# Kernel optimization log

Hardware: AMD Instinct MI355X
Metric: run time of the kernel (lower is better)

## Reference

```python
import jax, jax.numpy as jnp
import numpy as np

D = 2048
NUM_HEADS = 16
HEAD_DIM = D // NUM_HEADS
B, T = 4, 2048
NEG = -1e9


def setup_inputs() -> dict:
    key = jax.random.key(0)
    ks = jax.random.split(key, 6)
    X = jax.random.normal(ks[0], (B, T, D), dtype=jnp.float32)
    # additive causal mask, broadcast over batch and heads
    causal = jnp.tril(jnp.ones((T, T), dtype=jnp.float32))
    mask = jnp.where(causal == 1, 0.0, NEG)[None, None, :, :]
    scale = np.sqrt(2.0 / D).astype(np.float32)
    wq_w = jax.random.normal(ks[1], (D, D), dtype=jnp.float32) * scale
    wk_w = jax.random.normal(ks[2], (D, D), dtype=jnp.float32) * scale
    wv_w = jax.random.normal(ks[3], (D, D), dtype=jnp.float32) * scale
    wo_w = jax.random.normal(ks[4], (D, D), dtype=jnp.float32) * scale
    zeros = jnp.zeros((D,), dtype=jnp.float32)
    return {
        "X": X, "mask": mask,
        "wq_w": wq_w, "wq_b": zeros,
        "wk_w": wk_w, "wk_b": zeros,
        "wv_w": wv_w, "wv_b": zeros,
        "wo_w": wo_w, "wo_b": zeros,
    }


def reference(X, mask, wq_w, wq_b, wk_w, wk_b, wv_w, wv_b, wo_w, wo_b):
    b, t, d = X.shape
    # project and split heads: [b, h, t, hd]
    def proj(w, bias):
        return (X @ w + bias).reshape(b, t, NUM_HEADS, HEAD_DIM).transpose(0, 2, 1, 3)
    Q = proj(wq_w, wq_b)
    K = proj(wk_w, wk_b)
    V = proj(wv_w, wv_b)
    scores = jnp.einsum("bhqd,bhkd->bhqk", Q, K) / np.sqrt(HEAD_DIM).astype(X.dtype)
    scores = scores + mask
    A = jax.nn.softmax(scores, axis=-1)
    ctx = jnp.einsum("bhqk,bhkd->bhqd", A, V)  # [b, h, t, hd]
    ctx = ctx.transpose(0, 2, 1, 3).reshape(b, t, d)
    return ctx @ wo_w + wo_b
```

## Files before the change

### kernel.cpp

```cpp
#include <hip/hip_runtime.h>
#include <stdint.h>

#define DMODEL 2048
#define NH 16
#define HD 128
#define BATCH 4
#define SEQ 2048
#define MTOT (BATCH * SEQ)
#define LOG2E 1.44269504088896340736f

typedef __bf16 bf16x8 __attribute__((ext_vector_type(8)));
typedef float floatx4 __attribute__((ext_vector_type(4)));

__device__ __forceinline__ uint16_t f2b(float f) {
    union { float f; uint32_t i; } v; v.f = f;
    uint32_t r = v.i + 0x7fffu + ((v.i >> 16) & 1u);
    return (uint16_t)(r >> 16);
}

#define GLD16(gp, lp)                                                          \
    __builtin_amdgcn_global_load_lds(                                          \
        (__attribute__((address_space(1))) unsigned int*)(gp),                 \
        (__attribute__((address_space(3))) unsigned int*)(lp), 16, 0, 0)

#define WAITVMC(N) asm volatile("s_waitcnt vmcnt(" #N ")" ::: "memory")
#define WAITLGKM0                                                              \
    do {                                                                       \
        asm volatile("s_waitcnt lgkmcnt(0)" ::: "memory");                     \
        __builtin_amdgcn_sched_barrier(0);                                     \
    } while (0)

__global__ __launch_bounds__(256) void cvt_bf16(const float* __restrict__ in,
                                                uint16_t* __restrict__ out, int n) {
    const int i = (blockIdx.x * 256 + threadIdx.x) * 8;
    if (i >= n) return;
    const float4 a = *(const float4*)(in + i);
    const float4 b = *(const float4*)(in + i + 4);
    uint16_t v[8] __attribute__((aligned(16))) = {
        f2b(a.x), f2b(a.y), f2b(a.z), f2b(a.w),
        f2b(b.x), f2b(b.y), f2b(b.z), f2b(b.w)};
    *(uint4*)(out + i) = *(const uint4*)v;
}

__global__ __launch_bounds__(256) void tr_wf(const float* __restrict__ in,
                                             uint16_t* __restrict__ out) {
    __shared__ float t[64 * 69];
    const int tid = threadIdx.x;
    const int r0 = blockIdx.y * 64, c0 = blockIdx.x * 64;
    const int rr = tid >> 2, c16 = (tid & 3) << 4;
#pragma unroll
    for (int j = 0; j < 4; j++)
        *(float4*)&t[rr * 69 + c16 + j * 4] =
            *(const float4*)(in + (size_t)(r0 + rr) * DMODEL + c0 + c16 + j * 4);
    __syncthreads();
    const int oc = tid >> 2, r16 = (tid & 3) << 4;
    uint16_t v[16] __attribute__((aligned(16)));
#pragma unroll
    for (int j = 0; j < 16; j++) v[j] = f2b(t[(r16 + j) * 69 + oc]);
    uint16_t* o = out + (size_t)(c0 + oc) * DMODEL + r0 + r16;
    *(uint4*)o = *(const uint4*)v;
    *(uint4*)(o + 8) = *(const uint4*)(v + 8);
}

__global__ __launch_bounds__(512, 2) void gemm256(const uint16_t* __restrict__ A,
                                                  const uint16_t* __restrict__ Bt,
                                                  const float* __restrict__ bias,
                                                  void* __restrict__ Cout,
                                                  float scale, int mode, int tld) {
    __shared__ __attribute__((aligned(16))) uint16_t As[2][32 * 512];
    __shared__ __attribute__((aligned(16))) uint16_t Bs[2][32 * 512];

    const int tid = threadIdx.x, lane = tid & 63, w = tid >> 6;
    const int wr = w >> 2, wc = w & 3;
    const int col = lane & 15, quad = lane >> 4;

    const int nwg = gridDim.x, cpx = nwg >> 3;
    const int swz = ((int)blockIdx.x & 7) * cpx + ((int)blockIdx.x >> 3);
    const long m0 = (long)(swz >> 3) * 256;
    const long n0 = (long)(swz & 7) * 256;

    const uint16_t* Ab = A + (m0 + col) * (size_t)DMODEL + quad * 8;
    const uint16_t* Bb = Bt + (n0 + col) * (size_t)DMODEL + quad * 8;
    const int g0 = w * 2, g1 = w * 2 + 1;

#define STG_A(bf, kt, kk)                                                      \
    do {                                                                       \
        GLD16(Ab + (size_t)(g0 * 16) * DMODEL + (kt) * 64 + (kk) * 32,         \
              &As[bf][(g0 * 2 + (kk)) * 512]);                                 \
        GLD16(Ab + (size_t)(g1 * 16) * DMODEL + (kt) * 64 + (kk) * 32,         \
              &As[bf][(g1 * 2 + (kk)) * 512]);                                 \
    } while (0)
#define STG_B(bf, kt, kk)                                                      \
    do {                                                                       \
        GLD16(Bb + (size_t)(g0 * 16) * DMODEL + (kt) * 64 + (kk) * 32,         \
              &Bs[bf][(g0 * 2 + (kk)) * 512]);                                 \
        GLD16(Bb + (size_t)(g1 * 16) * DMODEL + (kt) * 64 + (kk) * 32,         \
              &Bs[bf][(g1 * 2 + (kk)) * 512]);                                 \
    } while (0)

    floatx4 acc[8][4];
#pragma unroll
    for (int m = 0; m < 8; m++)
#pragma unroll
        for (int n = 0; n < 4; n++) acc[m][n] = (floatx4){0.f, 0.f, 0.f, 0.f};

    const int NT = DMODEL / 64;
    STG_A(0, 0, 0); STG_B(0, 0, 0);
    STG_A(0, 0, 1); STG_B(0, 0, 1);
    STG_A(1, 1, 0); STG_B(1, 1, 0);
    WAITVMC(8);
    __builtin_amdgcn_s_barrier();

    bf16x8 afr[4], bfr[4];

#define PHASE(MS, KK, READB, STAGE_STMT, TAILW)                                \
    do {                                                                       \
        if (READB) {                                                           \
            _Pragma("unroll") for (int n = 0; n < 4; n++)                      \
                bfr[n] = *(const bf16x8*)&Bs[cur][((wc * 4 + n) * 2 + (KK)) *  \
                                                     512 + lane * 8];          \
        }                                                                      \
        _Pragma("unroll") for (int m = 0; m < 4; m++)                          \
            afr[m] = *(const bf16x8*)&As[cur][((wr * 8 + (MS)*4 + m) * 2 +     \
                                               (KK)) * 512 + lane * 8];        \
        STAGE_STMT;                                                            \
        __builtin_amdgcn_s_barrier();                                          \
        WAITLGKM0;                                                             \
        __builtin_amdgcn_s_setprio(1);                                         \
        _Pragma("unroll") for (int m = 0; m < 4; m++)                          \
            _Pragma("unroll") for (int n = 0; n < 4; n++)                      \
                acc[(MS)*4 + m][n] = __builtin_amdgcn_mfma_f32_16x16x32_bf16(  \
                    afr[m], bfr[n], acc[(MS)*4 + m][n], 0, 0, 0);              \
        __builtin_amdgcn_s_setprio(0);                                         \
        TAILW;                                                                 \
        __builtin_amdgcn_s_barrier();                                          \
    } while (0)

#pragma unroll 1
    for (int t = 0; t < NT; ++t) {
        const int cur = t & 1, nxt = cur ^ 1;
        PHASE(0, 0, 1, { if (t + 1 < NT) STG_A(nxt, t + 1, 1); }, {});
        PHASE(1, 0, 0, { if (t + 1 < NT) STG_B(nxt, t + 1, 1); },
              { if (t == NT - 1) { WAITVMC(0); } else { WAITVMC(8); } });
        PHASE(0, 1, 1, { if (t + 2 < NT) STG_A(cur, t + 2, 0); }, {});
        PHASE(1, 1, 0, { if (t + 2 < NT) STG_B(cur, t + 2, 0); },
              { if (t == NT - 2) { WAITVMC(2); }
                else if (t < NT - 2) { WAITVMC(8); } });
    }
#undef PHASE
#undef STG_A
#undef STG_B

    float bv[4];
#pragma unroll
    for (int n = 0; n < 4; n++) bv[n] = bias[n0 + wc * 64 + n * 16 + col];
#pragma unroll
    for (int m = 0; m < 8; m++) {
        const long row = m0 + wr * 128 + m * 16 + quad * 4;
#pragma unroll
        for (int n = 0; n < 4; n++) {
            const long cc = n0 + wc * 64 + n * 16 + col;
            if (mode == 2) {
                uint16_t tmp[4] __attribute__((aligned(8)));
#pragma unroll
                for (int r = 0; r < 4; r++)
                    tmp[r] = f2b((acc[m][n][r] + bv[n]) * scale);
                *(uint2*)&((uint16_t*)Cout)[(size_t)cc * tld + row] =
                    *(const uint2*)tmp;
            } else {
#pragma unroll
                for (int r = 0; r < 4; r++) {
                    const float v = (acc[m][n][r] + bv[n]) * scale;
                    const long idx = (row + r) * DMODEL + cc;
                    if (mode == 1) ((float*)Cout)[idx] = v;
                    else           ((uint16_t*)Cout)[idx] = f2b(v);
                }
            }
        }
    }
}

__global__ __launch_bounds__(256, 2) void gemm(const uint16_t* __restrict__ A,
                                               const uint16_t* __restrict__ Bt,
                                               const float* __restrict__ bias,
                                               void* __restrict__ Cout,
                                               float scale, int mode, int tld) {
    __shared__ __attribute__((aligned(16))) uint16_t As[128 * 32];
    __shared__ __attribute__((aligned(16))) uint16_t Bs[128 * 32];
    const int tid = threadIdx.x, lane = tid & 63, w = tid >> 6;
    const int wr = w >> 1, wc = w & 1;
    const int col = lane & 15, quad = lane >> 4;
    const long m0 = (long)blockIdx.y * 128, n0 = (long)blockIdx.x * 128;

    floatx4 acc[4][4];
#pragma unroll
    for (int i = 0; i < 4; i++)
#pragma unroll
        for (int j = 0; j < 4; j++) acc[i][j] = (floatx4){0.f, 0.f, 0.f, 0.f};

    const int srow = tid >> 2, sc = (tid & 3) << 3;
    const uint16_t* Ag0 = A + (m0 + srow) * DMODEL + sc;
    const uint16_t* Bg0 = Bt + (n0 + srow) * DMODEL + sc;
    const long rstep = (long)64 * DMODEL;
    uint16_t* AsW = &As[w * 512];
    uint16_t* BsW = &Bs[w * 512];

    for (int kt = 0; kt < DMODEL; kt += 32) {
        GLD16(Ag0 + kt, AsW);
        GLD16(Ag0 + rstep + kt, AsW + 2048);
        GLD16(Bg0 + kt, BsW);
        GLD16(Bg0 + rstep + kt, BsW + 2048);
        __syncthreads();
        bf16x8 af[4], bfr[4];
#pragma unroll
        for (int i = 0; i < 4; i++)
            af[i] = *(const bf16x8*)&As[(wr * 64 + i * 16 + col) * 32 + quad * 8];
#pragma unroll
        for (int j = 0; j < 4; j++)
            bfr[j] = *(const bf16x8*)&Bs[(wc * 64 + j * 16 + col) * 32 + quad * 8];
#pragma unroll
        for (int i = 0; i < 4; i++)
#pragma unroll
            for (int j = 0; j < 4; j++)
                acc[i][j] = __builtin_amdgcn_mfma_f32_16x16x32_bf16(af[i], bfr[j],
                                                                    acc[i][j], 0, 0, 0);
        __syncthreads();
    }

    float bv[4];
#pragma unroll
    for (int j = 0; j < 4; j++) bv[j] = bias[n0 + wc * 64 + j * 16 + col];
#pragma unroll
    for (int i = 0; i < 4; i++) {
        const long row = m0 + wr * 64 + i * 16 + quad * 4;
#pragma unroll
        for (int j = 0; j < 4; j++) {
            const long cc = n0 + wc * 64 + j * 16 + col;
            if (mode == 2) {
                uint16_t tmp[4] __attribute__((aligned(8)));
#pragma unroll
                for (int r = 0; r < 4; r++)
                    tmp[r] = f2b((acc[i][j][r] + bv[j]) * scale);
                *(uint2*)&((uint16_t*)Cout)[(size_t)cc * tld + row] =
                    *(const uint2*)tmp;
            } else {
#pragma unroll
                for (int r = 0; r < 4; r++) {
                    const float v = (acc[i][j][r] + bv[j]) * scale;
                    const long idx = (row + r) * DMODEL + cc;
                    if (mode == 1) ((float*)Cout)[idx] = v;
                    else           ((uint16_t*)Cout)[idx] = f2b(v);
                }
            }
        }
    }
}

__global__ __launch_bounds__(256, 2) void flash(uint16_t* __restrict__ QO,
                                                const uint16_t* __restrict__ Kp,
                                                const uint16_t* __restrict__ Vt,
                                                int vld) {
    __shared__ __attribute__((aligned(16))) uint16_t Ks[16 * 512];
    __shared__ __attribute__((aligned(16))) uint16_t Vs[16 * 512];
    __shared__ __attribute__((aligned(16))) uint16_t Ps[4][32 * 88];

    const int tid = threadIdx.x, lane = tid & 63, w = tid >> 6;
    const int col = lane & 15, quad = lane >> 4;
    const int h = blockIdx.y & 15, b = blockIdx.y >> 4;
    const size_t brow = (size_t)b * SEQ;

    const uint16_t* kbase = Kp + brow * DMODEL + h * HD;
    const uint16_t* vtbase = Vt + (size_t)(h * HD) * vld + brow;
    const uint16_t* kg0 = kbase + (size_t)(w * 16 + col) * DMODEL + quad * 8;
    const uint16_t* vg0 = vtbase + (size_t)(w * 32 + col) * vld + quad * 8;

    for (int half = 0; half < 2; ++half) {
        const int qi = half ? (int)blockIdx.x : (15 - (int)blockIdx.x);
        const int q0 = qi * 128;
        uint16_t* qbase = QO + (brow + q0 + w * 32) * DMODEL + h * HD;

        bf16x8 qf[2][4];
#pragma unroll
        for (int i = 0; i < 2; i++)
#pragma unroll
            for (int kk = 0; kk < 4; kk++)
                qf[i][kk] = *(const bf16x8*)(qbase + (size_t)(i * 16 + col) * DMODEL +
                                             kk * 32 + quad * 8);

        floatx4 accO[2][8];
#pragma unroll
        for (int i = 0; i < 2; i++)
#pragma unroll
            for (int jd = 0; jd < 8; jd++) accO[i][jd] = (floatx4){0.f, 0.f, 0.f, 0.f};
        float mrun[2][4], lrun[2][4];
#pragma unroll
        for (int i = 0; i < 2; i++)
#pragma unroll
            for (int r = 0; r < 4; r++) { mrun[i][r] = -1e30f; lrun[i][r] = 0.f; }

        const int nkt = 2 * qi + 2;

        uint4 kv[4], vv4[4];
        {
#pragma unroll
            for (int p = 0; p < 4; p++)
                kv[p] = *(const uint4*)(kg0 + p * 32);
#pragma unroll
            for (int s = 0; s < 2; s++)
#pragma unroll
                for (int k2 = 0; k2 < 2; k2++)
                    vv4[s * 2 + k2] =
                        *(const uint4*)(vg0 + (size_t)s * 16 * vld + k2 * 32);
        }

        for (int ki = 0; ki < nkt; ki++) {
            const int key0 = ki * 64;
#pragma unroll
            for (int p = 0; p < 4; p++)
                *(uint4*)&Ks[(w * 4 + p) * 512 + lane * 8] = kv[p];
#pragma unroll
            for (int s = 0; s < 2; s++)
#pragma unroll
                for (int k2 = 0; k2 < 2; k2++)
                    *(uint4*)&Vs[((w * 2 + s) * 2 + k2) * 512 + lane * 8] =
                        vv4[s * 2 + k2];
            __syncthreads();

            if (ki + 1 < nkt) {
                const size_t koff = (size_t)(key0 + 64);
#pragma unroll
                for (int p = 0; p < 4; p++)
                    kv[p] = *(const uint4*)(kg0 + koff * DMODEL + p * 32);
#pragma unroll
                for (int s = 0; s < 2; s++)
#pragma unroll
                    for (int k2 = 0; k2 < 2; k2++)
                        vv4[s * 2 + k2] = *(const uint4*)(vg0 + (size_t)s * 16 * vld +
                                                          koff + k2 * 32);
            }

            floatx4 s[2][4];
            __builtin_amdgcn_s_setprio(1);
#pragma unroll
            for (int i = 0; i < 2; i++)
#pragma unroll
                for (int jk = 0; jk < 4; jk++) {
                    floatx4 a = (floatx4){0.f, 0.f, 0.f, 0.f};
#pragma unroll
                    for (int kk = 0; kk < 4; kk++) {
                        bf16x8 bb = *(const bf16x8*)&Ks[(jk * 4 + kk) * 512 + lane * 8];
                        a = __builtin_amdgcn_mfma_f32_16x16x32_bf16(qf[i][kk], bb, a, 0, 0, 0);
                    }
                    s[i][jk] = a;
                }
            __builtin_amdgcn_s_setprio(0);

            if (key0 + 63 > q0 + w * 32) {
#pragma unroll
                for (int i = 0; i < 2; i++) {
                    const int qb = q0 + w * 32 + i * 16 + quad * 4;
#pragma unroll
                    for (int jk = 0; jk < 4; jk++) {
                        const int key = key0 + jk * 16 + col;
#pragma unroll
                        for (int r = 0; r < 4; r++)
                            if (key > qb + r) s[i][jk][r] = -1e30f;
                    }
                }
            }

            float alpha[2][4];
#pragma unroll
            for (int i = 0; i < 2; i++)
#pragma unroll
                for (int r = 0; r < 4; r++) {
                    float mx = s[i][0][r];
#pragma unroll
                    for (int jk = 1; jk < 4; jk++) mx = fmaxf(mx, s[i][jk][r]);
                    mx = fmaxf(mx, __shfl_xor(mx, 1, 64));
                    mx = fmaxf(mx, __shfl_xor(mx, 2, 64));
                    mx = fmaxf(mx, __shfl_xor(mx, 4, 64));
                    mx = fmaxf(mx, __shfl_xor(mx, 8, 64));
                    mx = fmaxf(mx, mrun[i][r]);
                    alpha[i][r] = exp2f((mrun[i][r] - mx) * LOG2E);
                    mrun[i][r] = mx;
                }
#pragma unroll
            for (int i = 0; i < 2; i++)
#pragma unroll
                for (int r = 0; r < 4; r++) {
                    float psum = 0.f;
#pragma unroll
                    for (int jk = 0; jk < 4; jk++) {
                        const float p = exp2f((s[i][jk][r] - mrun[i][r]) * LOG2E);
                        psum += p;
                        Ps[w][(i * 16 + quad * 4 + r) * 88 + jk * 16 + col] = f2b(p);
                    }
                    lrun[i][r] = lrun[i][r] * alpha[i][r] + psum;
                }
#pragma unroll
            for (int i = 0; i < 2; i++)
#pragma unroll
                for (int jd = 0; jd < 8; jd++)
#pragma unroll
                    for (int r = 0; r < 4; r++) accO[i][jd][r] *= alpha[i][r];

            bf16x8 pf[2][2];
#pragma unroll
            for (int i = 0; i < 2; i++)
#pragma unroll
                for (int k2 = 0; k2 < 2; k2++)
                    pf[i][k2] = *(const bf16x8*)&Ps[w][(i * 16 + col) * 88 + k2 * 32 + quad * 8];
            __builtin_amdgcn_s_setprio(1);
#pragma unroll
            for (int jd = 0; jd < 8; jd++)
#pragma unroll
                for (int k2 = 0; k2 < 2; k2++) {
                    bf16x8 vvv = *(const bf16x8*)&Vs[(jd * 2 + k2) * 512 + lane * 8];
#pragma unroll
                    for (int i = 0; i < 2; i++)
                        accO[i][jd] = __builtin_amdgcn_mfma_f32_16x16x32_bf16(pf[i][k2], vvv,
                                                                              accO[i][jd], 0, 0, 0);
                }
            __builtin_amdgcn_s_setprio(0);
            __syncthreads();
        }

        float inv[2][4];
#pragma unroll
        for (int i = 0; i < 2; i++)
#pragma unroll
            for (int r = 0; r < 4; r++) {
                float l = lrun[i][r];
                l += __shfl_xor(l, 1, 64);
                l += __shfl_xor(l, 2, 64);
                l += __shfl_xor(l, 4, 64);
                l += __shfl_xor(l, 8, 64);
                inv[i][r] = 1.0f / l;
            }
#pragma unroll
        for (int i = 0; i < 2; i++)
#pragma unroll
            for (int jd = 0; jd < 8; jd++)
#pragma unroll
                for (int r = 0; r < 4; r++)
                    qbase[(size_t)(i * 16 + quad * 4 + r) * DMODEL + jd * 16 + col] =
                        f2b(accO[i][jd][r] * inv[i][r]);
    }
}

extern "C" void kernel_launch(void* const* d_in, const int* in_sizes, int n_in,
                              void* d_out, int out_size, void* d_ws, size_t ws_size,
                              hipStream_t stream) {
    const float* X   = (const float*)d_in[0];
    float*       msk = (float*)d_in[1];
    const float* wq  = (const float*)d_in[2];
    const float* wqb = (const float*)d_in[3];
    const float* wk  = (const float*)d_in[4];
    const float* wkb = (const float*)d_in[5];
    const float* wv  = (const float*)d_in[6];
    const float* wvb = (const float*)d_in[7];
    const float* wo  = (const float*)d_in[8];
    const float* wob = (const float*)d_in[9];
    float* out = (float*)d_out;

    char* ws = (char*)d_ws;
    const size_t MB = 1ull << 20;
    dim3 tb(256), tb512(512), gT(32, 32);
    const float qs = 0.08838834764831845f;

    if (ws_size >= 136 * MB) {
        uint16_t* Xb = (uint16_t*)(ws);
        uint16_t* Qb = (uint16_t*)(ws + 32 * MB);
        uint16_t* Kb = (uint16_t*)(ws + 64 * MB);
        uint16_t* Vb = (uint16_t*)(ws + 96 * MB);
        uint16_t* Wt = (uint16_t*)(ws + 128 * MB);
        dim3 g256((MTOT / 256) * (DMODEL / 256));
        dim3 gF(8, 64);
        cvt_bf16<<<8192, tb, 0, stream>>>(X, Xb, MTOT * DMODEL);
        tr_wf<<<gT, tb, 0, stream>>>(wq, Wt);
        gemm256<<<g256, tb512, 0, stream>>>(Xb, Wt, wqb, Qb, qs, 0, 0);
        tr_wf<<<gT, tb, 0, stream>>>(wk, Wt);
        gemm256<<<g256, tb512, 0, stream>>>(Xb, Wt, wkb, Kb, 1.0f, 0, 0);
        tr_wf<<<gT, tb, 0, stream>>>(wv, Wt);
        gemm256<<<g256, tb512, 0, stream>>>(Xb, Wt, wvb, Vb, 1.0f, 2, MTOT);
        flash<<<gF, tb, 0, stream>>>(Qb, Kb, Vb, MTOT);
        tr_wf<<<gT, tb, 0, stream>>>(wo, Wt);
        gemm256<<<g256, tb512, 0, stream>>>(Qb, Wt, wob, out, 1.0f, 1, 0);
    } else {
        uint16_t* Xb = (uint16_t*)(ws);
        uint16_t* Qb = (uint16_t*)(ws + 8 * MB);
        uint16_t *Kb, *Vb, *Wt;
        if (ws_size >= 40 * MB) {
            Kb = (uint16_t*)(ws + 16 * MB);
            Vb = (uint16_t*)(ws + 24 * MB);
            Wt = (uint16_t*)(ws + 32 * MB);
        } else {
            Kb = (uint16_t*)msk;
            Vb = Kb + (size_t)SEQ * DMODEL;
            Wt = (uint16_t*)(ws + 16 * MB);
        }
        dim3 gG(16, 16), gF(8, 16);
        for (int b = 0; b < BATCH; b++) {
            const float* Xf = X + (size_t)b * SEQ * DMODEL;
            float* Ob = out + (size_t)b * SEQ * DMODEL;
            cvt_bf16<<<2048, tb, 0, stream>>>(Xf, Xb, SEQ * DMODEL);
            tr_wf<<<gT, tb, 0, stream>>>(wq, Wt);
            gemm<<<gG, tb, 0, stream>>>(Xb, Wt, wqb, Qb, qs, 0, 0);
            tr_wf<<<gT, tb, 0, stream>>>(wk, Wt);
            gemm<<<gG, tb, 0, stream>>>(Xb, Wt, wkb, Kb, 1.0f, 0, 0);
            tr_wf<<<gT, tb, 0, stream>>>(wv, Wt);
            gemm<<<gG, tb, 0, stream>>>(Xb, Wt, wvb, Vb, 1.0f, 2, SEQ);
            flash<<<gF, tb, 0, stream>>>(Qb, Kb, Vb, SEQ);
            tr_wf<<<gT, tb, 0, stream>>>(wo, Wt);
            gemm<<<gG, tb, 0, stream>>>(Qb, Wt, wob, Ob, 1.0f, 1, 0);
        }
    }

    (void)in_sizes; (void)n_in; (void)out_size;
}
```

Baseline: 714.2 us.

## Restructure flash attention: transposed S, register-shuffled P, async LDS loads

The flash kernel now computes S transposed (K as the A operand), so each lane holds one query column. Softmax reductions shrink to two cross-quad shuffles, and P is repacked into MFMA A-fragments with v_cvt_pk_bf16 and lane shuffles instead of round-tripping through shared memory. K/V tiles are loaded directly into LDS with global_load_lds, which drops the register prefetch. Each block now handles one query tile instead of a paired light/heavy tile, so the grid doubles and occupancy is raised to 3 blocks per SM. The risks are load imbalance from the causal work skew, and losing the overlap that the register prefetch gave, since the loads are now exposed right before the barrier.

```diff
diff --git a/kernel.cpp b/kernel.cpp
--- a/kernel.cpp
+++ b/kernel.cpp
@@ -16,6 +16,12 @@
     union { float f; uint32_t i; } v; v.f = f;
     uint32_t r = v.i + 0x7fffu + ((v.i >> 16) & 1u);
     return (uint16_t)(r >> 16);
+}
+
+__device__ __forceinline__ uint32_t cvtpk(float lo, float hi) {
+    uint32_t r;
+    asm("v_cvt_pk_bf16_f32 %0, %1, %2" : "=v"(r) : "v"(lo), "v"(hi));
+    return r;
 }
 
 #define GLD16(gp, lp)                                                          \
@@ -256,197 +262,186 @@
     }
 }
 
-__global__ __launch_bounds__(256, 2) void flash(uint16_t* __restrict__ QO,
+__global__ __launch_bounds__(256, 3) void flash(uint16_t* __restrict__ QO,
                                                 const uint16_t* __restrict__ Kp,
                                                 const uint16_t* __restrict__ Vt,
                                                 int vld) {
     __shared__ __attribute__((aligned(16))) uint16_t Ks[16 * 512];
     __shared__ __attribute__((aligned(16))) uint16_t Vs[16 * 512];
-    __shared__ __attribute__((aligned(16))) uint16_t Ps[4][32 * 88];
 
     const int tid = threadIdx.x, lane = tid & 63, w = tid >> 6;
     const int col = lane & 15, quad = lane >> 4;
     const int h = blockIdx.y & 15, b = blockIdx.y >> 4;
     const size_t brow = (size_t)b * SEQ;
+    const int qi = 15 - (int)blockIdx.x;
+    const int q0 = qi * 128;
 
     const uint16_t* kbase = Kp + brow * DMODEL + h * HD;
     const uint16_t* vtbase = Vt + (size_t)(h * HD) * vld + brow;
-    const uint16_t* kg0 = kbase + (size_t)(w * 16 + col) * DMODEL + quad * 8;
+    uint16_t* qbase = QO + (brow + q0 + w * 32) * DMODEL + h * HD;
+
+    const uint16_t* kg = kbase + (size_t)(w * 16 + col) * DMODEL + quad * 8;
     const uint16_t* vg0 = vtbase + (size_t)(w * 32 + col) * vld + quad * 8;
-
-    for (int half = 0; half < 2; ++half) {
-        const int qi = half ? (int)blockIdx.x : (15 - (int)blockIdx.x);
-        const int q0 = qi * 128;
-        uint16_t* qbase = QO + (brow + q0 + w * 32) * DMODEL + h * HD;
-
-        bf16x8 qf[2][4];
+    const uint16_t* vg1 = vtbase + (size_t)(w * 32 + 16 + col) * vld + quad * 8;
+
+    bf16x8 qf[2][4];
+#pragma unroll
+    for (int i = 0; i < 2; i++)
+#pragma unroll
+        for (int kk = 0; kk < 4; kk++)
+            qf[i][kk] = *(const bf16x8*)(qbase + (size_t)(i * 16 + col) * DMODEL +
+                                         kk * 32 + quad * 8);
+
+    floatx4 accO[2][8];
+#pragma unroll
+    for (int i = 0; i < 2; i++)
+#pragma unroll
+        for (int jd = 0; jd < 8; jd++) accO[i][jd] = (floatx4){0.f, 0.f, 0.f, 0.f};
+    float mrun[2] = {-1e30f, -1e30f}, lrun[2] = {0.f, 0.f};
+
+    const int nkt = 2 * qi + 2;
+    for (int ki = 0; ki < nkt; ki++) {
+        const size_t key0 = (size_t)ki * 64;
+#pragma unroll
+        for (int p = 0; p < 4; p++)
+            GLD16(kg + key0 * DMODEL + p * 32, &Ks[(w * 4 + p) * 512]);
+#pragma unroll
+        for (int k2 = 0; k2 < 2; k2++) {
+            GLD16(vg0 + key0 + k2 * 32, &Vs[((w * 2 + 0) * 2 + k2) * 512]);
+            GLD16(vg1 + key0 + k2 * 32, &Vs[((w * 2 + 1) * 2 + k2) * 512]);
+        }
+        __syncthreads();
+
+        floatx4 s[2][4];
 #pragma unroll
         for (int i = 0; i < 2; i++)
 #pragma unroll
-            for (int kk = 0; kk < 4; kk++)
-                qf[i][kk] = *(const bf16x8*)(qbase + (size_t)(i * 16 + col) * DMODEL +
-                                             kk * 32 + quad * 8);
-
-        floatx4 accO[2][8];
+            for (int jk = 0; jk < 4; jk++) s[i][jk] = (floatx4){0.f, 0.f, 0.f, 0.f};
+        __builtin_amdgcn_s_setprio(1);
+#pragma unroll
+        for (int jk = 0; jk < 4; jk++)
+#pragma unroll
+            for (int kk = 0; kk < 4; kk++) {
+                const bf16x8 bb = *(const bf16x8*)&Ks[(jk * 4 + kk) * 512 + lane * 8];
+#pragma unroll
+                for (int i = 0; i < 2; i++)
+                    s[i][jk] = __builtin_amdgcn_mfma_f32_16x16x32_bf16(bb, qf[i][kk],
+                                                                       s[i][jk], 0, 0, 0);
+            }
+        __builtin_amdgcn_s_setprio(0);
+
+        if ((int)key0 + 63 > q0 + w * 32) {
+#pragma unroll
+            for (int i = 0; i < 2; i++) {
+                const int qg = q0 + w * 32 + i * 16 + col;
+#pragma unroll
+                for (int jk = 0; jk < 4; jk++)
+#pragma unroll
+                    for (int r = 0; r < 4; r++) {
+                        const int key = (int)key0 + jk * 16 + quad * 4 + r;
+                        if (key > qg) s[i][jk][r] = -1e30f;
+                    }
+            }
+        }
+
+        float abr[2][4];
+#pragma unroll
+        for (int i = 0; i < 2; i++) {
+            float mx = s[i][0][0];
+#pragma unroll
+            for (int jk = 0; jk < 4; jk++)
+#pragma unroll
+                for (int r = 0; r < 4; r++) mx = fmaxf(mx, s[i][jk][r]);
+            mx = fmaxf(mx, __shfl_xor(mx, 16, 64));
+            mx = fmaxf(mx, __shfl_xor(mx, 32, 64));
+            mx = fmaxf(mx, mrun[i]);
+            const float al = exp2f((mrun[i] - mx) * LOG2E);
+            mrun[i] = mx;
+            float ps = 0.f;
+#pragma unroll
+            for (int jk = 0; jk < 4; jk++)
+#pragma unroll
+                for (int r = 0; r < 4; r++) {
+                    const float p = exp2f((s[i][jk][r] - mx) * LOG2E);
+                    s[i][jk][r] = p;
+                    ps += p;
+                }
+            lrun[i] = lrun[i] * al + ps;
+#pragma unroll
+            for (int r = 0; r < 4; r++) abr[i][r] = __shfl(al, quad * 4 + r, 64);
+        }
 #pragma unroll
         for (int i = 0; i < 2; i++)
 #pragma unroll
-            for (int jd = 0; jd < 8; jd++) accO[i][jd] = (floatx4){0.f, 0.f, 0.f, 0.f};
-        float mrun[2][4], lrun[2][4];
+            for (int jd = 0; jd < 8; jd++)
+#pragma unroll
+                for (int r = 0; r < 4; r++) accO[i][jd][r] *= abr[i][r];
+
+        bf16x8 pa[2][2];
 #pragma unroll
         for (int i = 0; i < 2; i++)
 #pragma unroll
-            for (int r = 0; r < 4; r++) { mrun[i][r] = -1e30f; lrun[i][r] = 0.f; }
-
-        const int nkt = 2 * qi + 2;
-
-        uint4 kv[4], vv4[4];
-        {
-#pragma unroll
-            for (int p = 0; p < 4; p++)
-                kv[p] = *(const uint4*)(kg0 + p * 32);
-#pragma unroll
-            for (int s = 0; s < 2; s++)
-#pragma unroll
-                for (int k2 = 0; k2 < 2; k2++)
-                    vv4[s * 2 + k2] =
-                        *(const uint4*)(vg0 + (size_t)s * 16 * vld + k2 * 32);
-        }
-
-        for (int ki = 0; ki < nkt; ki++) {
-            const int key0 = ki * 64;
-#pragma unroll
-            for (int p = 0; p < 4; p++)
-                *(uint4*)&Ks[(w * 4 + p) * 512 + lane * 8] = kv[p];
-#pragma unroll
-            for (int s = 0; s < 2; s++)
-#pragma unroll
-                for (int k2 = 0; k2 < 2; k2++)
-                    *(uint4*)&Vs[((w * 2 + s) * 2 + k2) * 512 + lane * 8] =
-                        vv4[s * 2 + k2];
-            __syncthreads();
-
-            if (ki + 1 < nkt) {
-                const size_t koff = (size_t)(key0 + 64);
-#pragma unroll
-                for (int p = 0; p < 4; p++)
-                    kv[p] = *(const uint4*)(kg0 + koff * DMODEL + p * 32);
-#pragma unroll
-                for (int s = 0; s < 2; s++)
-#pragma unroll
-                    for (int k2 = 0; k2 < 2; k2++)
-                        vv4[s * 2 + k2] = *(const uint4*)(vg0 + (size_t)s * 16 * vld +
-                                                          koff + k2 * 32);
+            for (int k2 = 0; k2 < 2; k2++) {
+                const int jlo = 2 * k2, jhi = jlo + 1;
+                const uint32_t c0l = cvtpk(s[i][jlo][0], s[i][jlo][1]);
+                const uint32_t c1l = cvtpk(s[i][jlo][2], s[i][jlo][3]);
+                const uint32_t c0h = cvtpk(s[i][jhi][0], s[i][jhi][1]);
+                const uint32_t c1h = cvtpk(s[i][jhi][2], s[i][jhi][3]);
+                const uint32_t n0l = __shfl_xor(c0l, 16, 64);
+                const uint32_t n1l = __shfl_xor(c1l, 16, 64);
+                const uint32_t n0h = __shfl_xor(c0h, 16, 64);
+                const uint32_t n1h = __shfl_xor(c1h, 16, 64);
+                const bool oddq = (quad & 1) != 0;
+                uint4 blo = oddq ? make_uint4(n0l, n1l, c0l, c1l)
+                                 : make_uint4(c0l, c1l, n0l, n1l);
+                uint4 bhi = oddq ? make_uint4(n0h, n1h, c0h, c1h)
+                                 : make_uint4(c0h, c1h, n0h, n1h);
+                uint4 snd = (quad < 2) ? bhi : blo;
+                uint4 rcv;
+                rcv.x = __shfl_xor(snd.x, 32, 64);
+                rcv.y = __shfl_xor(snd.y, 32, 64);
+                rcv.z = __shfl_xor(snd.z, 32, 64);
+                rcv.w = __shfl_xor(snd.w, 32, 64);
+                uint4 kee = (quad >= 2) ? bhi : blo;
+                uint4 sel = (quad == 1 || quad == 2) ? rcv : kee;
+                union { uint4 u; bf16x8 v; } cv;
+                cv.u = sel;
+                pa[i][k2] = cv.v;
             }
 
-            floatx4 s[2][4];
-            __builtin_amdgcn_s_setprio(1);
-#pragma unroll
-            for (int i = 0; i < 2; i++)
-#pragma unroll
-                for (int jk = 0; jk < 4; jk++) {
-                    floatx4 a = (floatx4){0.f, 0.f, 0.f, 0.f};
-#pragma unroll
-                    for (int kk = 0; kk < 4; kk++) {
-                        bf16x8 bb = *(const bf16x8*)&Ks[(jk * 4 + kk) * 512 + lane * 8];
-                        a = __builtin_amdgcn_mfma_f32_16x16x32_bf16(qf[i][kk], bb, a, 0, 0, 0);
-                    }
-                    s[i][jk] = a;
-                }
-            __builtin_amdgcn_s_setprio(0);
-
-            if (key0 + 63 > q0 + w * 32) {
-#pragma unroll
-                for (int i = 0; i < 2; i++) {
-                    const int qb = q0 + w * 32 + i * 16 + quad * 4;
-#pragma unroll
-                    for (int jk = 0; jk < 4; jk++) {
-                        const int key = key0 + jk * 16 + col;
-#pragma unroll
-                        for (int r = 0; r < 4; r++)
-                            if (key > qb + r) s[i][jk][r] = -1e30f;
-                    }
-                }
+        __builtin_amdgcn_s_setprio(1);
+#pragma unroll
+        for (int jd = 0; jd < 8; jd++)
+#pragma unroll
+            for (int k2 = 0; k2 < 2; k2++) {
+                const bf16x8 vvv = *(const bf16x8*)&Vs[(jd * 2 + k2) * 512 + lane * 8];
+#pragma unroll
+                for (int i = 0; i < 2; i++)
+                    accO[i][jd] = __builtin_amdgcn_mfma_f32_16x16x32_bf16(pa[i][k2], vvv,
+                                                                          accO[i][jd], 0, 0, 0);
             }
-
-            float alpha[2][4];
-#pragma unroll
-            for (int i = 0; i < 2; i++)
-#pragma unroll
-                for (int r = 0; r < 4; r++) {
-                    float mx = s[i][0][r];
-#pragma unroll
-                    for (int jk = 1; jk < 4; jk++) mx = fmaxf(mx, s[i][jk][r]);
-                    mx = fmaxf(mx, __shfl_xor(mx, 1, 64));
-                    mx = fmaxf(mx, __shfl_xor(mx, 2, 64));
-                    mx = fmaxf(mx, __shfl_xor(mx, 4, 64));
-                    mx = fmaxf(mx, __shfl_xor(mx, 8, 64));
-                    mx = fmaxf(mx, mrun[i][r]);
-                    alpha[i][r] = exp2f((mrun[i][r] - mx) * LOG2E);
-                    mrun[i][r] = mx;
-                }
-#pragma unroll
-            for (int i = 0; i < 2; i++)
-#pragma unroll
-                for (int r = 0; r < 4; r++) {
-                    float psum = 0.f;
-#pragma unroll
-                    for (int jk = 0; jk < 4; jk++) {
-                        const float p = exp2f((s[i][jk][r] - mrun[i][r]) * LOG2E);
-                        psum += p;
-                        Ps[w][(i * 16 + quad * 4 + r) * 88 + jk * 16 + col] = f2b(p);
-                    }
-                    lrun[i][r] = lrun[i][r] * alpha[i][r] + psum;
-                }
-#pragma unroll
-            for (int i = 0; i < 2; i++)
-#pragma unroll
-                for (int jd = 0; jd < 8; jd++)
-#pragma unroll
-                    for (int r = 0; r < 4; r++) accO[i][jd][r] *= alpha[i][r];
-
-            bf16x8 pf[2][2];
-#pragma unroll
-            for (int i = 0; i < 2; i++)
-#pragma unroll
-                for (int k2 = 0; k2 < 2; k2++)
-                    pf[i][k2] = *(const bf16x8*)&Ps[w][(i * 16 + col) * 88 + k2 * 32 + quad * 8];
-            __builtin_amdgcn_s_setprio(1);
-#pragma unroll
-            for (int jd = 0; jd < 8; jd++)
-#pragma unroll
-                for (int k2 = 0; k2 < 2; k2++) {
-                    bf16x8 vvv = *(const bf16x8*)&Vs[(jd * 2 + k2) * 512 + lane * 8];
-#pragma unroll
-                    for (int i = 0; i < 2; i++)
-                        accO[i][jd] = __builtin_amdgcn_mfma_f32_16x16x32_bf16(pf[i][k2], vvv,
-                                                                              accO[i][jd], 0, 0, 0);
-                }
-            __builtin_amdgcn_s_setprio(0);
-            __syncthreads();
-        }
-
-        float inv[2][4];
-#pragma unroll
-        for (int i = 0; i < 2; i++)
-#pragma unroll
-            for (int r = 0; r < 4; r++) {
-                float l = lrun[i][r];
-                l += __shfl_xor(l, 1, 64);
-                l += __shfl_xor(l, 2, 64);
-                l += __shfl_xor(l, 4, 64);
-                l += __shfl_xor(l, 8, 64);
-                inv[i][r] = 1.0f / l;
-            }
-#pragma unroll
-        for (int i = 0; i < 2; i++)
-#pragma unroll
-            for (int jd = 0; jd < 8; jd++)
-#pragma unroll
-                for (int r = 0; r < 4; r++)
-                    qbase[(size_t)(i * 16 + quad * 4 + r) * DMODEL + jd * 16 + col] =
-                        f2b(accO[i][jd][r] * inv[i][r]);
-    }
+        __builtin_amdgcn_s_setprio(0);
+        __syncthreads();
+    }
+
+    float ibr[2][4];
+#pragma unroll
+    for (int i = 0; i < 2; i++) {
+        float l = lrun[i];
+        l += __shfl_xor(l, 16, 64);
+        l += __shfl_xor(l, 32, 64);
+        const float iv = 1.0f / l;
+#pragma unroll
+        for (int r = 0; r < 4; r++) ibr[i][r] = __shfl(iv, quad * 4 + r, 64);
+    }
+#pragma unroll
+    for (int i = 0; i < 2; i++)
+#pragma unroll
+        for (int jd = 0; jd < 8; jd++)
+#pragma unroll
+            for (int r = 0; r < 4; r++)
+                qbase[(size_t)(i * 16 + quad * 4 + r) * DMODEL + jd * 16 + col] =
+                    f2b(accO[i][jd][r] * ibr[i][r]);
 }
 
 extern "C" void kernel_launch(void* const* d_in, const int* in_sizes, int n_in,
@@ -476,7 +471,7 @@
         uint16_t* Vb = (uint16_t*)(ws + 96 * MB);
         uint16_t* Wt = (uint16_t*)(ws + 128 * MB);
         dim3 g256((MTOT / 256) * (DMODEL / 256));
-        dim3 gF(8, 64);
+        dim3 gF(16, 64);
         cvt_bf16<<<8192, tb, 0, stream>>>(X, Xb, MTOT * DMODEL);
         tr_wf<<<gT, tb, 0, stream>>>(wq, Wt);
         gemm256<<<g256, tb512, 0, stream>>>(Xb, Wt, wqb, Qb, qs, 0, 0);
@@ -500,7 +495,7 @@
             Vb = Kb + (size_t)SEQ * DMODEL;
             Wt = (uint16_t*)(ws + 16 * MB);
         }
-        dim3 gG(16, 16), gF(8, 16);
+        dim3 gG(16, 16), gF(16, 16);
         for (int b = 0; b < BATCH; b++) {
             const float* Xf = X + (size_t)b * SEQ * DMODEL;
             float* Ob = out + (size_t)b * SEQ * DMODEL;
```

After: 899.1 us. 25.9% more time.
